# Kernel tuning notes

Hardware: AMD Instinct MI355X
Metric: run time of the kernel (lower is better)

## Reference

```python
import jax, jax.numpy as jnp
import numpy as np
import math

B, N, M, D = 8, 2048, 2048, 512

def setup_inputs() -> dict:
    key = jax.random.key(0)
    ks = jax.random.split(key, 12)
    s = 1.0 / math.sqrt(D)
    return {
        "query_xyz": jax.random.normal(ks[0], (B, N, 3), jnp.float32),
        "query_feat": jax.random.normal(ks[1], (B, N, D), jnp.float32),
        "key_xyz": jax.random.normal(ks[2], (B, M, 3), jnp.float32),
        "key_feat": jax.random.normal(ks[3], (B, M, D), jnp.float32),
        "Wq": jax.random.normal(ks[4], (D, D), jnp.float32) * s,
        "bq": jnp.zeros((D,), jnp.float32),
        "Wk": jax.random.normal(ks[5], (D, D), jnp.float32) * s,
        "bk": jnp.zeros((D,), jnp.float32),
        "Wv": jax.random.normal(ks[6], (D, D), jnp.float32) * s,
        "bv": jnp.zeros((D,), jnp.float32),
        "Wo": jax.random.normal(ks[7], (D, D), jnp.float32) * s,
        "bo": jnp.zeros((D,), jnp.float32),
        "ln_g": jnp.ones((D,), jnp.float32),
        "ln_b": jnp.zeros((D,), jnp.float32),
    }

def reference(query_xyz, query_feat, key_xyz, key_feat,
              Wq, bq, Wk, bk, Wv, bv, Wo, bo, ln_g, ln_b):
    d = query_feat.shape[-1]
    # projections (torch Linear: x @ W.T + b)
    Q = jnp.einsum('bnd,ed->bne', query_feat, Wq) + bq
    K = jnp.einsum('bmd,ed->bme', key_feat, Wk) + bk
    V = jnp.einsum('bmd,ed->bme', key_feat, Wv) + bv
    scores = jnp.einsum('bnd,bmd->bnm', Q, K) / jnp.sqrt(jnp.float32(d))
    # pairwise euclidean distance via (||q||^2 + ||k||^2 - 2 q.k), avoids BxNxMx3
    qn = jnp.sum(query_xyz * query_xyz, axis=-1)  # [B,N]
    kn = jnp.sum(key_xyz * key_xyz, axis=-1)      # [B,M]
    d2 = qn[:, :, None] + kn[:, None, :] - 2.0 * jnp.einsum('bnc,bmc->bnm', query_xyz, key_xyz)
    dist = jnp.sqrt(jnp.maximum(d2, 1e-12))
    # distance bias: log(exp(-2*dist) + 1e-8)
    scores = scores + jnp.log(jnp.exp(-dist * 2.0) + 1e-8)
    attn = jax.nn.softmax(scores, axis=-1)
    # dropout is identity in eval mode
    attended = jnp.einsum('bnm,bme->bne', attn, V)
    out = jnp.einsum('bne,fe->bnf', attended, Wo) + bo
    x = query_feat + out
    # LayerNorm (eps=1e-5)
    mu = jnp.mean(x, axis=-1, keepdims=True)
    var = jnp.mean((x - mu) ** 2, axis=-1, keepdims=True)
    return (x - mu) * jax.lax.rsqrt(var + 1e-5) * ln_g + ln_b
```

## Files before the change

### kernel.cpp

```cpp
#include <hip/hip_runtime.h>

typedef __attribute__((ext_vector_type(8))) short short8;
typedef __attribute__((ext_vector_type(8))) unsigned short us8;
typedef __attribute__((ext_vector_type(4))) unsigned short us4;
typedef __attribute__((ext_vector_type(4))) float f32x4;

__device__ __forceinline__ float bf2f(unsigned short h) {
  return __uint_as_float(((unsigned int)h) << 16);
}
__device__ __forceinline__ unsigned short f2bf(float f) {
  unsigned int u = __float_as_uint(f);
  u += 0x7FFF + ((u >> 16) & 1);
  return (unsigned short)(u >> 16);
}

__device__ __forceinline__ void gload16(const void* g, void* l) {
  __builtin_amdgcn_global_load_lds(
      (const __attribute__((address_space(1))) unsigned int*)g,
      (__attribute__((address_space(3))) unsigned int*)l, 16, 0, 0);
}

#define BM 128
#define BN 128
#define BK 32

struct EpiParams {
  const float* bias;
  const float* aux0;
  const float* aux1;
  long  saux;
  float scale;
};

template<int EPI>
__global__ __launch_bounds__(256)
void gemm_bt(const unsigned short* __restrict__ A, const unsigned short* __restrict__ B,
             void* __restrict__ Cout, int Kd, int lda, int ldb, int ldc,
             long sA, long sB, long sC, EpiParams ep)
{
  __shared__ __attribute__((aligned(16))) char smem[16384];
  char* Al = smem;
  char* Bl = smem + 8192;

  const int t    = threadIdx.x;
  const int lane = t & 63;
  const int wid  = t >> 6;
  const int wr   = wid >> 1;
  const int wc   = wid & 1;
  const int tr   = lane & 15;
  const int tg   = lane >> 4;

  const int bz    = blockIdx.z;
  const int rbase = blockIdx.y * BM;
  const int cbase = blockIdx.x * BN;

  const unsigned short* Ab = A + (long)bz * sA;
  const unsigned short* Bb = B + (long)bz * sB;
  const char* Asrc = (const char*)(Ab + (long)rbase * lda);
  const char* Bsrc = (const char*)(Bb + (long)cbase * ldb);
  const long lda_b = (long)lda * 2;
  const long ldb_b = (long)ldb * 2;

  f32x4 acc[4][4] = {};

  for (int k0 = 0; k0 < Kd; k0 += BK) {
#pragma unroll
    for (int it = 0; it < 2; ++it) {
      const int boff = (it * 4 + wid) * 1024 + lane * 16;
      const int r  = boff >> 6;
      const int cb = boff & 63;
      gload16(Asrc + (long)r * lda_b + (k0 * 2 + cb), Al + (it * 4 + wid) * 1024);
      gload16(Bsrc + (long)r * ldb_b + (k0 * 2 + cb), Bl + (it * 4 + wid) * 1024);
    }
    __syncthreads();

    short8 af[4], bf[4];
#pragma unroll
    for (int m = 0; m < 4; ++m)
      af[m] = *(const short8*)(Al + ((wr * 64 + m * 16 + tr) * 32 + tg * 8) * 2);
#pragma unroll
    for (int n = 0; n < 4; ++n)
      bf[n] = *(const short8*)(Bl + ((wc * 64 + n * 16 + tr) * 32 + tg * 8) * 2);
#pragma unroll
    for (int m = 0; m < 4; ++m)
#pragma unroll
      for (int n = 0; n < 4; ++n)
        acc[m][n] = __builtin_amdgcn_mfma_f32_16x16x32_bf16(af[m], bf[n], acc[m][n], 0, 0, 0);
    __syncthreads();
  }

  if (EPI == 0) {
    unsigned short* C = (unsigned short*)Cout + (long)bz * sC;
#pragma unroll
    for (int n = 0; n < 4; ++n) {
      const int col = cbase + wc * 64 + n * 16 + tr;
      const float bv = ep.bias ? ep.bias[col] : 0.f;
#pragma unroll
      for (int m = 0; m < 4; ++m) {
#pragma unroll
        for (int i = 0; i < 4; ++i) {
          const int row = rbase + wr * 64 + m * 16 + tg * 4 + i;
          C[(long)row * ldc + col] = f2bf(acc[m][n][i] + bv);
        }
      }
    }
  } else if (EPI == 1) {
    unsigned short* C = (unsigned short*)Cout;
#pragma unroll
    for (int n = 0; n < 4; ++n) {
      const int col = cbase + wc * 64 + n * 16 + tr;
      const float bv = ep.bias ? ep.bias[col] : 0.f;
#pragma unroll
      for (int m = 0; m < 4; ++m) {
        const int row0 = rbase + wr * 64 + m * 16 + tg * 4;
        const int b  = row0 >> 11;
        const int ml = row0 & 2047;
        us4 v;
#pragma unroll
        for (int i = 0; i < 4; ++i) v[i] = f2bf(acc[m][n][i] + bv);
        *(us4*)(C + ((long)b * 512 + col) * 2048 + ml) = v;
      }
    }
  } else {
    float* C = (float*)Cout;
    const float* qf = ep.aux0;
#pragma unroll
    for (int n = 0; n < 4; ++n) {
      const int col = cbase + wc * 64 + n * 16 + tr;
      const float bv = ep.bias ? ep.bias[col] : 0.f;
#pragma unroll
      for (int m = 0; m < 4; ++m) {
#pragma unroll
        for (int i = 0; i < 4; ++i) {
          const int row = rbase + wr * 64 + m * 16 + tg * 4 + i;
          C[(long)row * 512 + col] = acc[m][n][i] + bv + qf[(long)row * 512 + col];
        }
      }
    }
  }
}

template<int EPI, int NWC>
__global__ __launch_bounds__(128 * NWC, 2)
void gemm_big(const unsigned short* __restrict__ A, const unsigned short* __restrict__ B,
              void* __restrict__ Cout, int Kd, int lda, int ldb, int ldc,
              long sA, long sB, long sC, int ntn, EpiParams ep)
{
  constexpr int T  = 128 * NWC;
  constexpr int NF = 128 / (NWC * 16);
  constexpr int RA = 16384 / (T * 16);
  constexpr int RB = 8192 / (T * 16);

  __shared__ __attribute__((aligned(16))) char smem[24576];
  char* Al = smem;
  char* Bl = smem + 16384;

  const int t    = threadIdx.x;
  const int lane = t & 63;
  const int wid  = t >> 6;
  const int wr   = wid / NWC;
  const int wc   = wid % NWC;
  const int tr   = lane & 15;
  const int tg   = lane >> 4;

  const int bz    = blockIdx.x;
  const int rbase = (blockIdx.y / ntn) * 256;
  const int cbase = (blockIdx.y % ntn) * 128;

  const unsigned short* Ab = A + (long)bz * sA;
  const unsigned short* Bb = B + (long)bz * sB;
  const char* Asrc = (const char*)(Ab + (long)rbase * lda);
  const char* Bsrc = (const char*)(Bb + (long)cbase * ldb);
  const long lda_b = (long)lda * 2;
  const long ldb_b = (long)ldb * 2;

  f32x4 acc[8][NF] = {};

  for (int k0 = 0; k0 < Kd; k0 += BK) {
#pragma unroll
    for (int r = 0; r < RA; ++r) {
      const int o = (r * T + t) * 16;
      gload16(Asrc + (long)(o >> 6) * lda_b + (k0 * 2 + (o & 63)),
              Al + (r * T + wid * 64) * 16);
    }
#pragma unroll
    for (int r = 0; r < RB; ++r) {
      const int o = (r * T + t) * 16;
      gload16(Bsrc + (long)(o >> 6) * ldb_b + (k0 * 2 + (o & 63)),
              Bl + (r * T + wid * 64) * 16);
    }
    __syncthreads();

    short8 af[8], bf[NF];
#pragma unroll
    for (int m = 0; m < 8; ++m)
      af[m] = *(const short8*)(Al + ((wr * 128 + m * 16 + tr) * 32 + tg * 8) * 2);
#pragma unroll
    for (int n = 0; n < NF; ++n)
      bf[n] = *(const short8*)(Bl + ((wc * (NF * 16) + n * 16 + tr) * 32 + tg * 8) * 2);
#pragma unroll
    for (int m = 0; m < 8; ++m)
#pragma unroll
      for (int n = 0; n < NF; ++n)
        acc[m][n] = __builtin_amdgcn_mfma_f32_16x16x32_bf16(af[m], bf[n], acc[m][n], 0, 0, 0);
    __syncthreads();
  }

  if (EPI == 0) {
    unsigned short* C = (unsigned short*)Cout + (long)bz * sC;
#pragma unroll
    for (int n = 0; n < NF; ++n) {
      const int col = cbase + wc * (NF * 16) + n * 16 + tr;
#pragma unroll
      for (int m = 0; m < 8; ++m) {
#pragma unroll
        for (int i = 0; i < 4; ++i) {
          const int row = rbase + wr * 128 + m * 16 + tg * 4 + i;
          C[(long)row * ldc + col] = f2bf(acc[m][n][i]);
        }
      }
    }
  } else {
    float* qs = (float*)smem;
    float* ks = (float*)smem + 768;
    {
      const float* q = ep.aux0 + (long)bz * ep.saux + (long)(rbase + t) * 3;
      qs[t * 3] = q[0]; qs[t * 3 + 1] = q[1]; qs[t * 3 + 2] = q[2];
      if (t < 128) {
        const float* k2 = ep.aux1 + (long)bz * ep.saux + (long)(cbase + t) * 3;
        ks[t * 3] = k2[0]; ks[t * 3 + 1] = k2[1]; ks[t * 3 + 2] = k2[2];
      }
    }
    __syncthreads();
    unsigned short* C = (unsigned short*)Cout + (long)bz * sC;
#pragma unroll
    for (int m = 0; m < 8; ++m) {
#pragma unroll
      for (int i = 0; i < 4; ++i) {
        const int rl = wr * 128 + m * 16 + tg * 4 + i;
        const float qx = qs[rl * 3], qy = qs[rl * 3 + 1], qz = qs[rl * 3 + 2];
#pragma unroll
        for (int n = 0; n < NF; ++n) {
          const int cl = wc * (NF * 16) + n * 16 + tr;
          const float dx = qx - ks[cl * 3];
          const float dy = qy - ks[cl * 3 + 1];
          const float dz = qz - ks[cl * 3 + 2];
          const float d2 = dx * dx + dy * dy + dz * dz;
          const float d  = sqrtf(fmaxf(d2, 1e-12f));
          const float bias = fmaxf(-2.f * d, -18.420680743952367f);
          C[(long)(rbase + rl) * ldc + (cbase + cl)] = f2bf(acc[m][n][i] * ep.scale + bias);
        }
      }
    }
  }
}

__global__ __launch_bounds__(256)
void softmax_rows(unsigned short* __restrict__ S)
{
  const int row  = blockIdx.x * 4 + (threadIdx.x >> 6);
  const int lane = threadIdx.x & 63;
  unsigned short* rp = S + (long)row * 2048;

  us8 v[4];
#pragma unroll
  for (int c = 0; c < 4; ++c) v[c] = *(const us8*)(rp + c * 512 + lane * 8);
  float f[32];
#pragma unroll
  for (int c = 0; c < 4; ++c)
#pragma unroll
    for (int j = 0; j < 8; ++j) f[c * 8 + j] = bf2f(v[c][j]);

  float mx = f[0];
#pragma unroll
  for (int i = 1; i < 32; ++i) mx = fmaxf(mx, f[i]);
#pragma unroll
  for (int off = 32; off; off >>= 1) mx = fmaxf(mx, __shfl_xor(mx, off, 64));

  float sum = 0.f;
#pragma unroll
  for (int i = 0; i < 32; ++i) { f[i] = __expf(f[i] - mx); sum += f[i]; }
#pragma unroll
  for (int off = 32; off; off >>= 1) sum += __shfl_xor(sum, off, 64);
  const float inv = 1.f / sum;

#pragma unroll
  for (int c = 0; c < 4; ++c) {
    us8 o;
#pragma unroll
    for (int j = 0; j < 8; ++j) o[j] = f2bf(f[c * 8 + j] * inv);
    *(us8*)(rp + c * 512 + lane * 8) = o;
  }
}

__global__ __launch_bounds__(256)
void ln_rows(const float* __restrict__ X, const float* __restrict__ g,
             const float* __restrict__ b, float* __restrict__ O)
{
  const int row  = blockIdx.x * 4 + (threadIdx.x >> 6);
  const int lane = threadIdx.x & 63;
  const float* xp = X + (long)row * 512;

  f32x4 v0 = *(const f32x4*)(xp + lane * 4);
  f32x4 v1 = *(const f32x4*)(xp + 256 + lane * 4);

  float s = 0.f;
#pragma unroll
  for (int j = 0; j < 4; ++j) s += v0[j] + v1[j];
#pragma unroll
  for (int off = 32; off; off >>= 1) s += __shfl_xor(s, off, 64);
  const float mu = s * (1.f / 512.f);

  float vs = 0.f;
#pragma unroll
  for (int j = 0; j < 4; ++j) {
    float d0 = v0[j] - mu, d1 = v1[j] - mu;
    vs += d0 * d0 + d1 * d1;
  }
#pragma unroll
  for (int off = 32; off; off >>= 1) vs += __shfl_xor(vs, off, 64);
  const float r = rsqrtf(vs * (1.f / 512.f) + 1e-5f);

  f32x4 g0 = *(const f32x4*)(g + lane * 4);
  f32x4 g1 = *(const f32x4*)(g + 256 + lane * 4);
  f32x4 b0 = *(const f32x4*)(b + lane * 4);
  f32x4 b1 = *(const f32x4*)(b + 256 + lane * 4);

  f32x4 o0, o1;
#pragma unroll
  for (int j = 0; j < 4; ++j) {
    o0[j] = (v0[j] - mu) * r * g0[j] + b0[j];
    o1[j] = (v1[j] - mu) * r * g1[j] + b1[j];
  }
  float* op = O + (long)row * 512;
  *(f32x4*)(op + lane * 4) = o0;
  *(f32x4*)(op + 256 + lane * 4) = o1;
}

__global__ __launch_bounds__(256)
void cvt_bf16(const float* __restrict__ src, unsigned short* __restrict__ dst, int nvec)
{
  const int i = blockIdx.x * blockDim.x + threadIdx.x;
  if (i >= nvec) return;
  const f32x4* s = (const f32x4*)src;
  f32x4 a = s[(long)i * 2];
  f32x4 c = s[(long)i * 2 + 1];
  us8 o;
#pragma unroll
  for (int j = 0; j < 4; ++j) { o[j] = f2bf(a[j]); o[4 + j] = f2bf(c[j]); }
  *(us8*)(dst + (long)i * 8) = o;
}

extern "C" void kernel_launch(void* const* d_in, const int* in_sizes, int n_in,
                              void* d_out, int out_size, void* d_ws, size_t ws_size,
                              hipStream_t stream)
{
  const float* qxyz  = (const float*)d_in[0];
  const float* qfeat = (const float*)d_in[1];
  const float* kxyz  = (const float*)d_in[2];
  const float* kfeat = (const float*)d_in[3];
  const float* Wq = (const float*)d_in[4];
  const float* bq = (const float*)d_in[5];
  const float* Wk = (const float*)d_in[6];
  const float* bk = (const float*)d_in[7];
  const float* Wv = (const float*)d_in[8];
  const float* bv = (const float*)d_in[9];
  const float* Wo = (const float*)d_in[10];
  const float* bo = (const float*)d_in[11];
  const float* lng = (const float*)d_in[12];
  const float* lnb = (const float*)d_in[13];

  const long SZ_FEAT = 16777216;
  char* ws = (char*)d_ws;
  if (ws_size < (size_t)153092096) return;

  unsigned short* XQ  = (unsigned short*)(ws);
  unsigned short* XK  = (unsigned short*)(ws + SZ_FEAT);
  unsigned short* QB  = (unsigned short*)(ws + 2 * SZ_FEAT);
  unsigned short* KB  = (unsigned short*)(ws + 3 * SZ_FEAT);
  unsigned short* VT  = (unsigned short*)(ws + 4 * SZ_FEAT);
  unsigned short* WQB = (unsigned short*)(ws + 5 * SZ_FEAT);
  unsigned short* WKB = WQB + 262144;
  unsigned short* WVB = WQB + 524288;
  unsigned short* WOB = WQB + 786432;
  unsigned short* SB  = (unsigned short*)(ws + 5 * SZ_FEAT + 2097152);
  unsigned short* ATT = QB;
  float* XRES = (float*)ws;

  cvt_bf16<<<4096, 256, 0, stream>>>(qfeat, XQ, 1048576);
  cvt_bf16<<<4096, 256, 0, stream>>>(kfeat, XK, 1048576);
  cvt_bf16<<<128, 256, 0, stream>>>(Wq, WQB, 32768);
  cvt_bf16<<<128, 256, 0, stream>>>(Wk, WKB, 32768);
  cvt_bf16<<<128, 256, 0, stream>>>(Wv, WVB, 32768);
  cvt_bf16<<<128, 256, 0, stream>>>(Wo, WOB, 32768);

  EpiParams e0{}; e0.bias = bq;
  gemm_bt<0><<<dim3(4, 128, 1), 256, 0, stream>>>(XQ, WQB, QB, 512, 512, 512, 512, 0, 0, 0, e0);
  EpiParams e1{}; e1.bias = bk;
  gemm_bt<0><<<dim3(4, 128, 1), 256, 0, stream>>>(XK, WKB, KB, 512, 512, 512, 512, 0, 0, 0, e1);
  EpiParams e2{}; e2.bias = bv;
  gemm_bt<1><<<dim3(4, 128, 1), 256, 0, stream>>>(XK, WVB, VT, 512, 512, 512, 0, 0, 0, 0, e2);

  EpiParams es{}; es.aux0 = qxyz; es.aux1 = kxyz; es.saux = 2048 * 3;
  es.scale = 0.044194173824159216f;
  gemm_big<2, 2><<<dim3(8, 128), 256, 0, stream>>>(QB, KB, SB, 512, 512, 512, 2048,
                                                   (long)2048 * 512, (long)2048 * 512,
                                                   (long)2048 * 2048, 16, es);

  softmax_rows<<<4096, 256, 0, stream>>>(SB);

  EpiParams ep{};
  gemm_big<0, 4><<<dim3(8, 32), 512, 0, stream>>>(SB, VT, ATT, 2048, 2048, 2048, 512,
                                                  (long)2048 * 2048, (long)512 * 2048,
                                                  (long)2048 * 512, 4, ep);

  EpiParams eo{}; eo.bias = bo; eo.aux0 = qfeat;
  gemm_bt<3><<<dim3(4, 128, 1), 256, 0, stream>>>(ATT, WOB, XRES, 512, 512, 512, 512, 0, 0, 0, eo);

  ln_rows<<<4096, 256, 0, stream>>>(XRES, lng, lnb, (float*)d_out);
}
```

Before: 279.5 us.

## Fuse softmax exp into score GEMM and defer normalization to PV epilogue

Removes the separate softmax pass. The score GEMM epilogue now computes exp(score - 5) directly, stores it as bf16 and atomically accumulates per-row sums into a workspace buffer. The PV GEMM epilogue divides by those sums. This drops a full read and write of the large score matrix. The K and V projection GEMMs are merged into one launch over a doubled column grid, and the six conversion launches are collapsed into two. The fixed offset instead of the true row maximum relies on scores staying within fp32 and bf16 exponent range, and it adds atomics and a memset.

```diff
diff --git a/kernel.cpp b/kernel.cpp
--- a/kernel.cpp
+++ b/kernel.cpp
@@ -28,6 +28,7 @@
   const float* bias;
   const float* aux0;
   const float* aux1;
+  const void*  aux2;
   long  saux;
   float scale;
 };
@@ -104,21 +105,38 @@
         }
       }
     }
-  } else if (EPI == 1) {
-    unsigned short* C = (unsigned short*)Cout;
-#pragma unroll
-    for (int n = 0; n < 4; ++n) {
-      const int col = cbase + wc * 64 + n * 16 + tr;
-      const float bv = ep.bias ? ep.bias[col] : 0.f;
-#pragma unroll
-      for (int m = 0; m < 4; ++m) {
-        const int row0 = rbase + wr * 64 + m * 16 + tg * 4;
-        const int b  = row0 >> 11;
-        const int ml = row0 & 2047;
-        us4 v;
-#pragma unroll
-        for (int i = 0; i < 4; ++i) v[i] = f2bf(acc[m][n][i] + bv);
-        *(us4*)(C + ((long)b * 512 + col) * 2048 + ml) = v;
+  } else if (EPI == 4) {
+    if (cbase < 512) {
+      unsigned short* C = (unsigned short*)Cout;
+#pragma unroll
+      for (int n = 0; n < 4; ++n) {
+        const int col = cbase + wc * 64 + n * 16 + tr;
+        const float bv = ep.bias[col];
+#pragma unroll
+        for (int m = 0; m < 4; ++m) {
+#pragma unroll
+          for (int i = 0; i < 4; ++i) {
+            const int row = rbase + wr * 64 + m * 16 + tg * 4 + i;
+            C[(long)row * 512 + col] = f2bf(acc[m][n][i] + bv);
+          }
+        }
+      }
+    } else {
+      unsigned short* C = (unsigned short*)ep.aux2;
+#pragma unroll
+      for (int n = 0; n < 4; ++n) {
+        const int e  = cbase - 512 + wc * 64 + n * 16 + tr;
+        const float bv = ep.aux1[e];
+#pragma unroll
+        for (int m = 0; m < 4; ++m) {
+          const int row0 = rbase + wr * 64 + m * 16 + tg * 4;
+          const int b  = row0 >> 11;
+          const int ml = row0 & 2047;
+          us4 v;
+#pragma unroll
+          for (int i = 0; i < 4; ++i) v[i] = f2bf(acc[m][n][i] + bv);
+          *(us4*)(C + ((long)b * 512 + e) * 2048 + ml) = v;
+        }
       }
     }
   } else {
@@ -208,15 +226,20 @@
 
   if (EPI == 0) {
     unsigned short* C = (unsigned short*)Cout + (long)bz * sC;
-#pragma unroll
-    for (int n = 0; n < NF; ++n) {
-      const int col = cbase + wc * (NF * 16) + n * 16 + tr;
-#pragma unroll
-      for (int m = 0; m < 8; ++m) {
+    const float* ls = (const float*)ep.aux2 + (long)bz * 2048 + rbase;
+#pragma unroll
+    for (int m = 0; m < 8; ++m) {
+      const f32x4 lv = *(const f32x4*)(ls + wr * 128 + m * 16 + tg * 4);
+      f32x4 inv;
+#pragma unroll
+      for (int i = 0; i < 4; ++i) inv[i] = 1.f / lv[i];
+#pragma unroll
+      for (int n = 0; n < NF; ++n) {
+        const int col = cbase + wc * (NF * 16) + n * 16 + tr;
 #pragma unroll
         for (int i = 0; i < 4; ++i) {
           const int row = rbase + wr * 128 + m * 16 + tg * 4 + i;
-          C[(long)row * ldc + col] = f2bf(acc[m][n][i]);
+          C[(long)row * ldc + col] = f2bf(acc[m][n][i] * inv[i]);
         }
       }
     }
@@ -233,10 +256,13 @@
     }
     __syncthreads();
     unsigned short* C = (unsigned short*)Cout + (long)bz * sC;
+    float* lrow = (float*)ep.aux2 + (long)bz * 2048 + rbase;
+    float ps[8][4];
 #pragma unroll
     for (int m = 0; m < 8; ++m) {
 #pragma unroll
       for (int i = 0; i < 4; ++i) {
+        ps[m][i] = 0.f;
         const int rl = wr * 128 + m * 16 + tg * 4 + i;
         const float qx = qs[rl * 3], qy = qs[rl * 3 + 1], qz = qs[rl * 3 + 2];
 #pragma unroll
@@ -248,48 +274,26 @@
           const float d2 = dx * dx + dy * dy + dz * dz;
           const float d  = sqrtf(fmaxf(d2, 1e-12f));
           const float bias = fmaxf(-2.f * d, -18.420680743952367f);
-          C[(long)(rbase + rl) * ldc + (cbase + cl)] = f2bf(acc[m][n][i] * ep.scale + bias);
-        }
-      }
-    }
-  }
-}
-
-__global__ __launch_bounds__(256)
-void softmax_rows(unsigned short* __restrict__ S)
-{
-  const int row  = blockIdx.x * 4 + (threadIdx.x >> 6);
-  const int lane = threadIdx.x & 63;
-  unsigned short* rp = S + (long)row * 2048;
-
-  us8 v[4];
-#pragma unroll
-  for (int c = 0; c < 4; ++c) v[c] = *(const us8*)(rp + c * 512 + lane * 8);
-  float f[32];
-#pragma unroll
-  for (int c = 0; c < 4; ++c)
-#pragma unroll
-    for (int j = 0; j < 8; ++j) f[c * 8 + j] = bf2f(v[c][j]);
-
-  float mx = f[0];
-#pragma unroll
-  for (int i = 1; i < 32; ++i) mx = fmaxf(mx, f[i]);
-#pragma unroll
-  for (int off = 32; off; off >>= 1) mx = fmaxf(mx, __shfl_xor(mx, off, 64));
-
-  float sum = 0.f;
-#pragma unroll
-  for (int i = 0; i < 32; ++i) { f[i] = __expf(f[i] - mx); sum += f[i]; }
-#pragma unroll
-  for (int off = 32; off; off >>= 1) sum += __shfl_xor(sum, off, 64);
-  const float inv = 1.f / sum;
-
-#pragma unroll
-  for (int c = 0; c < 4; ++c) {
-    us8 o;
-#pragma unroll
-    for (int j = 0; j < 8; ++j) o[j] = f2bf(f[c * 8 + j] * inv);
-    *(us8*)(rp + c * 512 + lane * 8) = o;
+          const float p = __expf(acc[m][n][i] * ep.scale + bias - 5.f);
+          ps[m][i] += p;
+          C[(long)(rbase + rl) * ldc + (cbase + cl)] = f2bf(p);
+        }
+      }
+    }
+#pragma unroll
+    for (int off = 1; off <= 8; off <<= 1)
+#pragma unroll
+      for (int m = 0; m < 8; ++m)
+#pragma unroll
+        for (int i = 0; i < 4; ++i)
+          ps[m][i] += __shfl_xor(ps[m][i], off, 64);
+    if (tr == 0) {
+#pragma unroll
+      for (int m = 0; m < 8; ++m)
+#pragma unroll
+        for (int i = 0; i < 4; ++i)
+          atomicAdd(&lrow[wr * 128 + m * 16 + tg * 4 + i], ps[m][i]);
+    }
   }
 }
 
@@ -338,17 +342,36 @@
 }
 
 __global__ __launch_bounds__(256)
-void cvt_bf16(const float* __restrict__ src, unsigned short* __restrict__ dst, int nvec)
-{
-  const int i = blockIdx.x * blockDim.x + threadIdx.x;
-  if (i >= nvec) return;
+void cvt_feat(const float* __restrict__ a, const float* __restrict__ b,
+              unsigned short* __restrict__ oa, unsigned short* __restrict__ ob)
+{
+  const float* src = blockIdx.y ? b : a;
+  unsigned short* dst = blockIdx.y ? ob : oa;
+  const long i = blockIdx.x * 256 + threadIdx.x;
   const f32x4* s = (const f32x4*)src;
-  f32x4 a = s[(long)i * 2];
-  f32x4 c = s[(long)i * 2 + 1];
+  f32x4 x = s[i * 2];
+  f32x4 y = s[i * 2 + 1];
   us8 o;
 #pragma unroll
-  for (int j = 0; j < 4; ++j) { o[j] = f2bf(a[j]); o[4 + j] = f2bf(c[j]); }
-  *(us8*)(dst + (long)i * 8) = o;
+  for (int j = 0; j < 4; ++j) { o[j] = f2bf(x[j]); o[4 + j] = f2bf(y[j]); }
+  *(us8*)(dst + i * 8) = o;
+}
+
+__global__ __launch_bounds__(256)
+void cvt_w(const float* __restrict__ w0, const float* __restrict__ w1,
+           const float* __restrict__ w2, const float* __restrict__ w3,
+           unsigned short* __restrict__ dst)
+{
+  const float* src = blockIdx.y == 0 ? w0 : blockIdx.y == 1 ? w1 : blockIdx.y == 2 ? w2 : w3;
+  unsigned short* d = dst + (long)blockIdx.y * 262144;
+  const long i = blockIdx.x * 256 + threadIdx.x;
+  const f32x4* s = (const f32x4*)src;
+  f32x4 x = s[i * 2];
+  f32x4 y = s[i * 2 + 1];
+  us8 o;
+#pragma unroll
+  for (int j = 0; j < 4; ++j) { o[j] = f2bf(x[j]); o[4 + j] = f2bf(y[j]); }
+  *(us8*)(d + i * 8) = o;
 }
 
 extern "C" void kernel_launch(void* const* d_in, const int* in_sizes, int n_in,
@@ -381,35 +404,29 @@
   unsigned short* VT  = (unsigned short*)(ws + 4 * SZ_FEAT);
   unsigned short* WQB = (unsigned short*)(ws + 5 * SZ_FEAT);
   unsigned short* WKB = WQB + 262144;
-  unsigned short* WVB = WQB + 524288;
   unsigned short* WOB = WQB + 786432;
   unsigned short* SB  = (unsigned short*)(ws + 5 * SZ_FEAT + 2097152);
   unsigned short* ATT = QB;
   float* XRES = (float*)ws;
-
-  cvt_bf16<<<4096, 256, 0, stream>>>(qfeat, XQ, 1048576);
-  cvt_bf16<<<4096, 256, 0, stream>>>(kfeat, XK, 1048576);
-  cvt_bf16<<<128, 256, 0, stream>>>(Wq, WQB, 32768);
-  cvt_bf16<<<128, 256, 0, stream>>>(Wk, WKB, 32768);
-  cvt_bf16<<<128, 256, 0, stream>>>(Wv, WVB, 32768);
-  cvt_bf16<<<128, 256, 0, stream>>>(Wo, WOB, 32768);
+  float* LSUM = (float*)(ws + SZ_FEAT);
+
+  cvt_feat<<<dim3(4096, 2), 256, 0, stream>>>(qfeat, kfeat, XQ, XK);
+  cvt_w<<<dim3(128, 4), 256, 0, stream>>>(Wq, Wk, Wv, Wo, WQB);
 
   EpiParams e0{}; e0.bias = bq;
   gemm_bt<0><<<dim3(4, 128, 1), 256, 0, stream>>>(XQ, WQB, QB, 512, 512, 512, 512, 0, 0, 0, e0);
-  EpiParams e1{}; e1.bias = bk;
-  gemm_bt<0><<<dim3(4, 128, 1), 256, 0, stream>>>(XK, WKB, KB, 512, 512, 512, 512, 0, 0, 0, e1);
-  EpiParams e2{}; e2.bias = bv;
-  gemm_bt<1><<<dim3(4, 128, 1), 256, 0, stream>>>(XK, WVB, VT, 512, 512, 512, 0, 0, 0, 0, e2);
-
-  EpiParams es{}; es.aux0 = qxyz; es.aux1 = kxyz; es.saux = 2048 * 3;
+  EpiParams e1{}; e1.bias = bk; e1.aux1 = bv; e1.aux2 = VT;
+  gemm_bt<4><<<dim3(8, 128, 1), 256, 0, stream>>>(XK, WKB, KB, 512, 512, 512, 512, 0, 0, 0, e1);
+
+  hipMemsetAsync(LSUM, 0, 8 * 2048 * sizeof(float), stream);
+
+  EpiParams es{}; es.aux0 = qxyz; es.aux1 = kxyz; es.aux2 = LSUM; es.saux = 2048 * 3;
   es.scale = 0.044194173824159216f;
   gemm_big<2, 2><<<dim3(8, 128), 256, 0, stream>>>(QB, KB, SB, 512, 512, 512, 2048,
                                                    (long)2048 * 512, (long)2048 * 512,
                                                    (long)2048 * 2048, 16, es);
 
-  softmax_rows<<<4096, 256, 0, stream>>>(SB);
-
-  EpiParams ep{};
+  EpiParams ep{}; ep.aux2 = LSUM;
   gemm_big<0, 4><<<dim3(8, 32), 512, 0, stream>>>(SB, VT, ATT, 2048, 2048, 2048, 512,
                                                   (long)2048 * 2048, (long)512 * 2048,
                                                   (long)2048 * 512, 4, ep);
```

Result: no change. 277.2 us (-0.8%).
